# Optimization experiments

Measured on AMD Instinct MI355X. Metric: run time of the kernel, lower is better.

## Reference

```python
import jax, jax.numpy as jnp
import numpy as np

N_NODES = 100000
N_EDGES = 1600000
N_FEAT = 32


def setup_inputs() -> dict:
    key = jax.random.key(0)
    k1, k2, k3, k4 = jax.random.split(key, 4)
    u = jax.random.normal(k1, (N_NODES, N_FEAT), dtype=jnp.float32)
    weights = jax.random.uniform(k2, (N_EDGES,), dtype=jnp.float32)
    row = jax.random.randint(k3, (N_EDGES,), 0, N_NODES)
    col = jax.random.randint(k4, (N_EDGES,), 0, N_NODES)
    edge_index = jnp.stack([row, col]).astype(jnp.int64)
    return {"u": u, "weights": weights, "edge_index": edge_index}


def reference(u, weights, edge_index):
    # row, col: [E]; u: [N, F]; weights: [E]
    row, col = edge_index[0], edge_index[1]
    diff = u[col] - u[row]                      # [E, F] edge gather + diff
    weighted_diff = weights[:, None] * diff     # [E, F]
    # scatter-add into node outputs (index_add_ on row)
    laplacian = jax.ops.segment_sum(weighted_diff, row, num_segments=u.shape[0])
    return laplacian
```

## Files before the change

### kernel.cpp

```cpp
#include <hip/hip_runtime.h>


#define NFEAT 32
#define BUCKET_BITS 7
#define HB 128
#define MAXNB 1024
#define CH 4096
#define HCAP 2560
#define HBLK 64

typedef float nfloat4 __attribute__((ext_vector_type(4)));
typedef unsigned int nuint2 __attribute__((ext_vector_type(2)));

__device__ __forceinline__ float4 nt_load_f4(const float4* p) {
    nfloat4 v = __builtin_nontemporal_load((const nfloat4*)p);
    return make_float4(v.x, v.y, v.z, v.w);
}
__device__ __forceinline__ void nt_store_f4(float4* p, float4 v) {
    nfloat4 t = {v.x, v.y, v.z, v.w};
    __builtin_nontemporal_store(t, (nfloat4*)p);
}
__device__ __forceinline__ uint2 nt_load_u2(const uint2* p) {
    nuint2 v = __builtin_nontemporal_load((const nuint2*)p);
    uint2 r; r.x = v.x; r.y = v.y; return r;
}

__device__ __forceinline__ int wave_incl_scan(int v, int lane) {
#pragma unroll
    for (int off = 1; off < 64; off <<= 1) {
        int t = __shfl_up(v, off, 64);
        if (lane >= off) v += t;
    }
    return v;
}

__global__ __launch_bounds__(512) void conv_hist_kernel(const float4* __restrict__ u4,
                                                        ushort4* __restrict__ ub, int n4,
                                                        const int* __restrict__ row,
                                                        int* __restrict__ hist_part,
                                                        int E, int convBlocks) {
    __shared__ int h[MAXNB];
    if ((int)blockIdx.x < convBlocks) {
        int i = blockIdx.x * 512 + threadIdx.x;
        if (i >= n4) return;
        float4 v = nt_load_f4(&u4[i]);
        ushort4 o;
        unsigned x;
        x = __float_as_uint(v.x); x += 0x7fffu + ((x >> 16) & 1u); o.x = (unsigned short)(x >> 16);
        x = __float_as_uint(v.y); x += 0x7fffu + ((x >> 16) & 1u); o.y = (unsigned short)(x >> 16);
        x = __float_as_uint(v.z); x += 0x7fffu + ((x >> 16) & 1u); o.z = (unsigned short)(x >> 16);
        x = __float_as_uint(v.w); x += 0x7fffu + ((x >> 16) & 1u); o.w = (unsigned short)(x >> 16);
        ub[i] = o;
    } else {
        int hb = blockIdx.x - convBlocks;
        for (int i = threadIdx.x; i < MAXNB; i += 512) h[i] = 0;
        __syncthreads();
        int stride = HBLK * 512;
        for (int e = hb * 512 + threadIdx.x; e < E; e += stride)
            atomicAdd(&h[__builtin_nontemporal_load(&row[e]) >> BUCKET_BITS], 1);
        __syncthreads();
        int* dst = hist_part + (size_t)hb * MAXNB;
        for (int i = threadIdx.x; i < MAXNB; i += 512) dst[i] = h[i];
    }
}

__global__ __launch_bounds__(512) void scan_offsets_kernel(const int* __restrict__ hist_part,
                                                           int* __restrict__ offsets,
                                                           int* __restrict__ cursor) {
    __shared__ int wsum[8];
    int t = threadIdx.x;
    int lane = t & 63, wid = t >> 6;
    int c0 = 0, c1 = 0;
    for (int p = 0; p < HBLK; ++p) {
        const int2* src = (const int2*)(hist_part + (size_t)p * MAXNB);
        int2 v = src[t];
        c0 += v.x; c1 += v.y;
    }
    int pair = c0 + c1;
    int incl = wave_incl_scan(pair, lane);
    if (lane == 63) wsum[wid] = incl;
    __syncthreads();
    int base = 0;
#pragma unroll
    for (int i = 0; i < 8; ++i) { int v = wsum[i]; if (i < wid) base += v; }
    incl += base;
    int excl = incl - pair;
    offsets[2 * t] = excl;
    cursor[2 * t] = excl;
    offsets[2 * t + 1] = excl + c0;
    cursor[2 * t + 1] = excl + c0;
    if (t == 511) offsets[MAXNB] = incl;
}

__global__ __launch_bounds__(512) void fill_sort_kernel(const int* __restrict__ row,
                                                        const int* __restrict__ col,
                                                        const float* __restrict__ w,
                                                        int* __restrict__ cursor,
                                                        uint2* __restrict__ csr,
                                                        int E) {
    __shared__ int hist[MAXNB];
    __shared__ int sc[MAXNB];
    __shared__ int gb0[MAXNB];
    __shared__ int wsum[8];
    __shared__ uint2 so[CH];
    __shared__ unsigned short sbs[CH];

    int tid = threadIdx.x;
    int lane = tid & 63, wid = tid >> 6;
    int lo = blockIdx.x * CH;
    int n = min(E - lo, CH);
    bool full = (n == CH);

    hist[tid] = 0;
    hist[tid + 512] = 0;
    __syncthreads();

    int rst[CH / 512];
    if (full) {
#pragma unroll
        for (int k = 0; k < CH / 512; ++k) {
            int r = __builtin_nontemporal_load(&row[lo + tid + k * 512]);
            rst[k] = r;
            atomicAdd(&hist[r >> BUCKET_BITS], 1);
        }
    } else {
        for (int i = tid; i < n; i += 512)
            atomicAdd(&hist[__builtin_nontemporal_load(&row[lo + i]) >> BUCKET_BITS], 1);
    }
    __syncthreads();

    int c0 = hist[2 * tid];
    int c1 = hist[2 * tid + 1];
    int pair = c0 + c1;
    int incl = wave_incl_scan(pair, lane);
    if (lane == 63) wsum[wid] = incl;
    __syncthreads();
    int base = 0;
#pragma unroll
    for (int i = 0; i < 8; ++i) { int v = wsum[i]; if (i < wid) base += v; }
    incl += base;
    int excl = incl - pair;
    sc[2 * tid] = excl;
    sc[2 * tid + 1] = excl + c0;

    int g0 = c0 ? atomicAdd(&cursor[2 * tid], c0) : 0;
    int g1 = c1 ? atomicAdd(&cursor[2 * tid + 1], c1) : 0;
    gb0[2 * tid] = g0;
    gb0[2 * tid + 1] = g1;
    hist[2 * tid] = g0;
    hist[2 * tid + 1] = g1;
    __syncthreads();

    if (full) {
#pragma unroll
        for (int k = 0; k < CH / 512; ++k) {
            int i = tid + k * 512;
            int r = rst[k];
            unsigned c = (unsigned)__builtin_nontemporal_load(&col[lo + i]);
            float wt = __builtin_nontemporal_load(&w[lo + i]);
            int b = r >> BUCKET_BITS;
            uint2 p;
            p.x = ((unsigned)(r & (HB - 1)) << 25) | c;
            p.y = __float_as_uint(wt);
            int d = atomicAdd(&hist[b], 1);
            int pos = sc[b] + (d - gb0[b]);
            so[pos] = p;
            sbs[pos] = (unsigned short)b;
        }
    } else {
        for (int i = tid; i < n; i += 512) {
            int r = __builtin_nontemporal_load(&row[lo + i]);
            unsigned c = (unsigned)__builtin_nontemporal_load(&col[lo + i]);
            float wt = __builtin_nontemporal_load(&w[lo + i]);
            int b = r >> BUCKET_BITS;
            uint2 p;
            p.x = ((unsigned)(r & (HB - 1)) << 25) | c;
            p.y = __float_as_uint(wt);
            int d = atomicAdd(&hist[b], 1);
            int pos = sc[b] + (d - gb0[b]);
            so[pos] = p;
            sbs[pos] = (unsigned short)b;
        }
    }
    __syncthreads();

    for (int i = tid; i < n; i += 512) {
        int b = sbs[i];
        csr[gb0[b] + (i - sc[b])] = so[i];
    }
}

__global__ __launch_bounds__(512) void node_half_kernel(const ushort4* __restrict__ ub,
                                                        const float4* __restrict__ u4,
                                                        const int* __restrict__ offsets,
                                                        const uint2* __restrict__ csr,
                                                        float4* __restrict__ out4, int N) {
    __shared__ uint2 se[HCAP];
    __shared__ int hist[HB];
    __shared__ int starts[HB + 1];
    __shared__ int sc[HB];

    int b = blockIdx.x;
    int tid = threadIdx.x;
    int start = offsets[b];
    int end = offsets[b + 1];
    int cnt = end - start;

    if (tid < HB) hist[tid] = 0;
    __syncthreads();

    if (cnt <= HCAP) {
        for (int i = start + tid; i < end; i += 512)
            atomicAdd(&hist[nt_load_u2(&csr[i]).x >> 25], 1);
        __syncthreads();
        int myc = (tid < HB) ? hist[tid] : 0;
        int lane = tid & 63;
        int incl = wave_incl_scan(myc, lane);
        if (lane == 63) sc[tid >> 6] = incl;
        __syncthreads();
        if (tid < HB) {
            if (tid >= 64) incl += sc[0];
            int excl = incl - myc;
            starts[tid] = excl;
            hist[tid] = excl;
            if (tid == HB - 1) starts[HB] = incl;
        }
        __syncthreads();
        for (int i = start + tid; i < end; i += 512) {
            uint2 p = nt_load_u2(&csr[i]);
            int pos = atomicAdd(&hist[p.x >> 25], 1);
            se[pos] = p;
        }
        __syncthreads();
        int wave = tid >> 6;
        int f4 = lane & 7;
        int slot = lane >> 3;
        for (int node = wave; node < HB; node += 8) {
            int s0 = starts[node];
            int s1 = starts[node + 1];
            float4 acc = make_float4(0.f, 0.f, 0.f, 0.f);
            float ws_ = 0.f;
            for (int i = s0 + slot; i < s1; i += 8) {
                uint2 p = se[i];
                int c = (int)(p.x & 0x01FFFFFFu);
                float wt = __uint_as_float(p.y);
                ushort4 us = ub[(size_t)c * 8 + f4];
                acc.x += wt * __uint_as_float((unsigned)us.x << 16);
                acc.y += wt * __uint_as_float((unsigned)us.y << 16);
                acc.z += wt * __uint_as_float((unsigned)us.z << 16);
                acc.w += wt * __uint_as_float((unsigned)us.w << 16);
                ws_ += wt;
            }
#pragma unroll
            for (int m = 8; m < 64; m <<= 1) {
                acc.x += __shfl_xor(acc.x, m, 64);
                acc.y += __shfl_xor(acc.y, m, 64);
                acc.z += __shfl_xor(acc.z, m, 64);
                acc.w += __shfl_xor(acc.w, m, 64);
                ws_   += __shfl_xor(ws_,   m, 64);
            }
            int glob = b * HB + node;
            if (slot == 0 && glob < N) {
                float4 ur = nt_load_f4(&u4[(size_t)glob * 8 + f4]);
                float4 o;
                o.x = acc.x - ws_ * ur.x;
                o.y = acc.y - ws_ * ur.y;
                o.z = acc.z - ws_ * ur.z;
                o.w = acc.w - ws_ * ur.w;
                nt_store_f4(&out4[(size_t)glob * 8 + f4], o);
            }
        }
    } else {
        float* tile = (float*)se;
        float* wsumf = (float*)sc;
        for (int i = tid; i < HB * NFEAT; i += 512) tile[i] = 0.f;
        if (tid < HB) wsumf[tid] = 0.f;
        __syncthreads();
        int f4 = tid & 7;
        for (int i = start + (tid >> 3); i < end; i += 64) {
            uint2 p = nt_load_u2(&csr[i]);
            int rl = (int)(p.x >> 25);
            int c = (int)(p.x & 0x01FFFFFFu);
            float wt = __uint_as_float(p.y);
            ushort4 us = ub[(size_t)c * 8 + f4];
            float* t = &tile[rl * NFEAT + f4 * 4];
            atomicAdd(t + 0, wt * __uint_as_float((unsigned)us.x << 16));
            atomicAdd(t + 1, wt * __uint_as_float((unsigned)us.y << 16));
            atomicAdd(t + 2, wt * __uint_as_float((unsigned)us.z << 16));
            atomicAdd(t + 3, wt * __uint_as_float((unsigned)us.w << 16));
            if (f4 == 0) atomicAdd(&wsumf[rl], wt);
        }
        __syncthreads();
#pragma unroll
        for (int pass = 0; pass < 2; ++pass) {
            int idx = pass * 512 + tid;
            int node = idx >> 3;
            int ff = idx & 7;
            int glob = b * HB + node;
            if (glob < N) {
                float4 ur = nt_load_f4(&u4[(size_t)glob * 8 + ff]);
                float ws_ = wsumf[node];
                const float* t = &tile[node * NFEAT + ff * 4];
                float4 o;
                o.x = t[0] - ws_ * ur.x;
                o.y = t[1] - ws_ * ur.y;
                o.z = t[2] - ws_ * ur.z;
                o.w = t[3] - ws_ * ur.w;
                nt_store_f4(&out4[(size_t)glob * 8 + ff], o);
            }
        }
    }
}


__global__ __launch_bounds__(256) void zero_out_kernel(float* __restrict__ out, int n) {
    int i = blockIdx.x * blockDim.x + threadIdx.x;
    if (i < n) out[i] = 0.0f;
}

__global__ __launch_bounds__(256) void scatter_lap_kernel(const float4* __restrict__ u4,
                                                          const float* __restrict__ w,
                                                          const int* __restrict__ row,
                                                          const int* __restrict__ col,
                                                          float* __restrict__ out, int n_edges) {
    int tid = blockIdx.x * blockDim.x + threadIdx.x;
    int e = tid >> 3;
    int f4 = tid & 7;
    if (e >= n_edges) return;
    int r = row[e];
    int c = col[e];
    float wt = w[e];
    float4 uc = u4[(size_t)c * 8 + f4];
    float4 ur = u4[(size_t)r * 8 + f4];
    float* o = out + (size_t)r * NFEAT + f4 * 4;
    atomicAdd(o + 0, wt * (uc.x - ur.x));
    atomicAdd(o + 1, wt * (uc.y - ur.y));
    atomicAdd(o + 2, wt * (uc.z - ur.z));
    atomicAdd(o + 3, wt * (uc.w - ur.w));
}

extern "C" void kernel_launch(void* const* d_in, const int* in_sizes, int n_in,
                              void* d_out, int out_size, void* d_ws, size_t ws_size,
                              hipStream_t stream) {
    const float* u = (const float*)d_in[0];
    const float* w = (const float*)d_in[1];
    const int* ei = (const int*)d_in[2];
    float* out = (float*)d_out;

    const int E = in_sizes[1];
    const int N = out_size / NFEAT;
    const int* row = ei;
    const int* col = ei + E;

    const int NBH = (N + HB - 1) >> BUCKET_BITS;

    const size_t histPartOff = 0;
    const size_t histPartBytes = ((size_t)HBLK * MAXNB * 4 + 255) & ~(size_t)255;
    const size_t offsetsOff = histPartOff + histPartBytes;
    const size_t offsetsBytes = ((size_t)(MAXNB + 1) * 4 + 255) & ~(size_t)255;
    const size_t cursorOff = offsetsOff + offsetsBytes;
    const size_t cursorBytes = ((size_t)MAXNB * 4 + 255) & ~(size_t)255;
    const size_t csrOff = cursorOff + cursorBytes;
    const size_t csrBytes = ((size_t)E * 8 + 255) & ~(size_t)255;
    const size_t ubOff = csrOff + csrBytes;
    const size_t ubBytes = ((size_t)N * NFEAT * 2 + 255) & ~(size_t)255;
    const size_t totalWs = ubOff + ubBytes;

    if (ws_size < totalWs || NBH > MAXNB - 1) {
        zero_out_kernel<<<(out_size + 255) / 256, 256, 0, stream>>>(out, out_size);
        long long threads_total = (long long)E * 8;
        scatter_lap_kernel<<<(unsigned)((threads_total + 255) / 256), 256, 0, stream>>>(
            (const float4*)u, w, row, col, out, E);
        return;
    }

    char* ws = (char*)d_ws;
    int* hist_part = (int*)(ws + histPartOff);
    int* offsets = (int*)(ws + offsetsOff);
    int* cursor = (int*)(ws + cursorOff);
    uint2* csr = (uint2*)(ws + csrOff);
    ushort4* ub = (ushort4*)(ws + ubOff);

    int n4 = N * (NFEAT / 4);
    int convBlocks = (n4 + 511) / 512;
    conv_hist_kernel<<<convBlocks + HBLK, 512, 0, stream>>>((const float4*)u, ub, n4,
                                                            row, hist_part, E, convBlocks);

    scan_offsets_kernel<<<1, 512, 0, stream>>>(hist_part, offsets, cursor);

    const int nChunks = (E + CH - 1) / CH;
    fill_sort_kernel<<<nChunks, 512, 0, stream>>>(row, col, w, cursor, csr, E);

    node_half_kernel<<<NBH, 512, 0, stream>>>(ub, (const float4*)u, offsets, csr,
                                              (float4*)out, N);
}
```

Measured before the change: 172.5 us.

## Fold offset scan and bf16 conversion into fill kernel, cache CSR slice in LDS

Drops the single-block scan kernel. Every fill_sort block now sums the 64 partial histograms and scans them redundantly to get global bucket offsets, and uses zeroed ticket counters in place of a precomputed cursor. The fp32-to-bf16 conversion of u moves from the histogram launch into the fill kernel's prologue, split evenly across its blocks. The node kernel stages its CSR slice in shared memory so the edge records are read from global memory once instead of twice, at the cost of doubling that kernel's LDS use and each fill block re-reading 256KB of partial histograms.

```diff
diff --git a/kernel.cpp b/kernel.cpp
--- a/kernel.cpp
+++ b/kernel.cpp
@@ -34,74 +34,41 @@
     return v;
 }
 
-__global__ __launch_bounds__(512) void conv_hist_kernel(const float4* __restrict__ u4,
-                                                        ushort4* __restrict__ ub, int n4,
-                                                        const int* __restrict__ row,
-                                                        int* __restrict__ hist_part,
-                                                        int E, int convBlocks) {
+__global__ __launch_bounds__(512) void hist_kernel(const int* __restrict__ row,
+                                                   int* __restrict__ hist_part,
+                                                   int* __restrict__ ticket,
+                                                   int E) {
     __shared__ int h[MAXNB];
-    if ((int)blockIdx.x < convBlocks) {
-        int i = blockIdx.x * 512 + threadIdx.x;
-        if (i >= n4) return;
-        float4 v = nt_load_f4(&u4[i]);
-        ushort4 o;
-        unsigned x;
-        x = __float_as_uint(v.x); x += 0x7fffu + ((x >> 16) & 1u); o.x = (unsigned short)(x >> 16);
-        x = __float_as_uint(v.y); x += 0x7fffu + ((x >> 16) & 1u); o.y = (unsigned short)(x >> 16);
-        x = __float_as_uint(v.z); x += 0x7fffu + ((x >> 16) & 1u); o.z = (unsigned short)(x >> 16);
-        x = __float_as_uint(v.w); x += 0x7fffu + ((x >> 16) & 1u); o.w = (unsigned short)(x >> 16);
-        ub[i] = o;
-    } else {
-        int hb = blockIdx.x - convBlocks;
-        for (int i = threadIdx.x; i < MAXNB; i += 512) h[i] = 0;
-        __syncthreads();
-        int stride = HBLK * 512;
-        for (int e = hb * 512 + threadIdx.x; e < E; e += stride)
-            atomicAdd(&h[__builtin_nontemporal_load(&row[e]) >> BUCKET_BITS], 1);
-        __syncthreads();
-        int* dst = hist_part + (size_t)hb * MAXNB;
-        for (int i = threadIdx.x; i < MAXNB; i += 512) dst[i] = h[i];
-    }
-}
-
-__global__ __launch_bounds__(512) void scan_offsets_kernel(const int* __restrict__ hist_part,
-                                                           int* __restrict__ offsets,
-                                                           int* __restrict__ cursor) {
-    __shared__ int wsum[8];
-    int t = threadIdx.x;
-    int lane = t & 63, wid = t >> 6;
-    int c0 = 0, c1 = 0;
-    for (int p = 0; p < HBLK; ++p) {
-        const int2* src = (const int2*)(hist_part + (size_t)p * MAXNB);
-        int2 v = src[t];
-        c0 += v.x; c1 += v.y;
-    }
-    int pair = c0 + c1;
-    int incl = wave_incl_scan(pair, lane);
-    if (lane == 63) wsum[wid] = incl;
-    __syncthreads();
-    int base = 0;
-#pragma unroll
-    for (int i = 0; i < 8; ++i) { int v = wsum[i]; if (i < wid) base += v; }
-    incl += base;
-    int excl = incl - pair;
-    offsets[2 * t] = excl;
-    cursor[2 * t] = excl;
-    offsets[2 * t + 1] = excl + c0;
-    cursor[2 * t + 1] = excl + c0;
-    if (t == 511) offsets[MAXNB] = incl;
+    int hb = blockIdx.x;
+    if (hb == 0) {
+        ticket[threadIdx.x] = 0;
+        ticket[threadIdx.x + 512] = 0;
+    }
+    for (int i = threadIdx.x; i < MAXNB; i += 512) h[i] = 0;
+    __syncthreads();
+    int stride = HBLK * 512;
+    for (int e = hb * 512 + threadIdx.x; e < E; e += stride)
+        atomicAdd(&h[__builtin_nontemporal_load(&row[e]) >> BUCKET_BITS], 1);
+    __syncthreads();
+    int* dst = hist_part + (size_t)hb * MAXNB;
+    for (int i = threadIdx.x; i < MAXNB; i += 512) dst[i] = h[i];
 }
 
 __global__ __launch_bounds__(512) void fill_sort_kernel(const int* __restrict__ row,
                                                         const int* __restrict__ col,
                                                         const float* __restrict__ w,
-                                                        int* __restrict__ cursor,
+                                                        const int* __restrict__ hist_part,
+                                                        int* __restrict__ ticket,
+                                                        int* __restrict__ offsets,
                                                         uint2* __restrict__ csr,
-                                                        int E) {
+                                                        const float4* __restrict__ u4,
+                                                        ushort4* __restrict__ ub,
+                                                        int n4, int E) {
     __shared__ int hist[MAXNB];
     __shared__ int sc[MAXNB];
     __shared__ int gb0[MAXNB];
-    __shared__ int wsum[8];
+    __shared__ int wsumL[8];
+    __shared__ int wsumG[8];
     __shared__ uint2 so[CH];
     __shared__ unsigned short sbs[CH];
 
@@ -111,6 +78,22 @@
     int n = min(E - lo, CH);
     bool full = (n == CH);
 
+    {
+        int per = (n4 + (int)gridDim.x - 1) / (int)gridDim.x;
+        int cb = blockIdx.x * per;
+        int ce = min(n4, cb + per);
+        for (int i = cb + tid; i < ce; i += 512) {
+            float4 v = nt_load_f4(&u4[i]);
+            ushort4 o;
+            unsigned x;
+            x = __float_as_uint(v.x); x += 0x7fffu + ((x >> 16) & 1u); o.x = (unsigned short)(x >> 16);
+            x = __float_as_uint(v.y); x += 0x7fffu + ((x >> 16) & 1u); o.y = (unsigned short)(x >> 16);
+            x = __float_as_uint(v.z); x += 0x7fffu + ((x >> 16) & 1u); o.z = (unsigned short)(x >> 16);
+            x = __float_as_uint(v.w); x += 0x7fffu + ((x >> 16) & 1u); o.w = (unsigned short)(x >> 16);
+            ub[i] = o;
+        }
+    }
+
     hist[tid] = 0;
     hist[tid + 512] = 0;
     __syncthreads();
@@ -127,24 +110,44 @@
         for (int i = tid; i < n; i += 512)
             atomicAdd(&hist[__builtin_nontemporal_load(&row[lo + i]) >> BUCKET_BITS], 1);
     }
+
+    int c0g = 0, c1g = 0;
+    for (int p = 0; p < HBLK; ++p) {
+        int2 v = ((const int2*)(hist_part + (size_t)p * MAXNB))[tid];
+        c0g += v.x; c1g += v.y;
+    }
     __syncthreads();
 
     int c0 = hist[2 * tid];
     int c1 = hist[2 * tid + 1];
-    int pair = c0 + c1;
-    int incl = wave_incl_scan(pair, lane);
-    if (lane == 63) wsum[wid] = incl;
-    __syncthreads();
-    int base = 0;
-#pragma unroll
-    for (int i = 0; i < 8; ++i) { int v = wsum[i]; if (i < wid) base += v; }
-    incl += base;
-    int excl = incl - pair;
-    sc[2 * tid] = excl;
-    sc[2 * tid + 1] = excl + c0;
-
-    int g0 = c0 ? atomicAdd(&cursor[2 * tid], c0) : 0;
-    int g1 = c1 ? atomicAdd(&cursor[2 * tid + 1], c1) : 0;
+    int pairL = c0 + c1;
+    int pairG = c0g + c1g;
+    int inclL = wave_incl_scan(pairL, lane);
+    int inclG = wave_incl_scan(pairG, lane);
+    if (lane == 63) { wsumL[wid] = inclL; wsumG[wid] = inclG; }
+    __syncthreads();
+    int baseL = 0, baseG = 0;
+#pragma unroll
+    for (int i = 0; i < 8; ++i) {
+        int vl = wsumL[i], vg = wsumG[i];
+        if (i < wid) { baseL += vl; baseG += vg; }
+    }
+    inclL += baseL;
+    inclG += baseG;
+    int exclL = inclL - pairL;
+    sc[2 * tid] = exclL;
+    sc[2 * tid + 1] = exclL + c0;
+    int gE0 = inclG - pairG;
+    int gE1 = gE0 + c0g;
+
+    if (blockIdx.x == 0) {
+        offsets[2 * tid] = gE0;
+        offsets[2 * tid + 1] = gE1;
+        if (tid == 511) offsets[MAXNB] = inclG;
+    }
+
+    int g0 = gE0 + (c0 ? atomicAdd(&ticket[2 * tid], c0) : 0);
+    int g1 = gE1 + (c1 ? atomicAdd(&ticket[2 * tid + 1], c1) : 0);
     gb0[2 * tid] = g0;
     gb0[2 * tid + 1] = g1;
     hist[2 * tid] = g0;
@@ -195,6 +198,7 @@
                                                         const int* __restrict__ offsets,
                                                         const uint2* __restrict__ csr,
                                                         float4* __restrict__ out4, int N) {
+    __shared__ uint2 sin_[HCAP];
     __shared__ uint2 se[HCAP];
     __shared__ int hist[HB];
     __shared__ int starts[HB + 1];
@@ -210,8 +214,11 @@
     __syncthreads();
 
     if (cnt <= HCAP) {
-        for (int i = start + tid; i < end; i += 512)
-            atomicAdd(&hist[nt_load_u2(&csr[i]).x >> 25], 1);
+        for (int i = start + tid; i < end; i += 512) {
+            uint2 p = nt_load_u2(&csr[i]);
+            sin_[i - start] = p;
+            atomicAdd(&hist[p.x >> 25], 1);
+        }
         __syncthreads();
         int myc = (tid < HB) ? hist[tid] : 0;
         int lane = tid & 63;
@@ -226,8 +233,8 @@
             if (tid == HB - 1) starts[HB] = incl;
         }
         __syncthreads();
-        for (int i = start + tid; i < end; i += 512) {
-            uint2 p = nt_load_u2(&csr[i]);
+        for (int j = tid; j < cnt; j += 512) {
+            uint2 p = sin_[j];
             int pos = atomicAdd(&hist[p.x >> 25], 1);
             se[pos] = p;
         }
@@ -358,9 +365,9 @@
     const size_t histPartBytes = ((size_t)HBLK * MAXNB * 4 + 255) & ~(size_t)255;
     const size_t offsetsOff = histPartOff + histPartBytes;
     const size_t offsetsBytes = ((size_t)(MAXNB + 1) * 4 + 255) & ~(size_t)255;
-    const size_t cursorOff = offsetsOff + offsetsBytes;
-    const size_t cursorBytes = ((size_t)MAXNB * 4 + 255) & ~(size_t)255;
-    const size_t csrOff = cursorOff + cursorBytes;
+    const size_t ticketOff = offsetsOff + offsetsBytes;
+    const size_t ticketBytes = ((size_t)MAXNB * 4 + 255) & ~(size_t)255;
+    const size_t csrOff = ticketOff + ticketBytes;
     const size_t csrBytes = ((size_t)E * 8 + 255) & ~(size_t)255;
     const size_t ubOff = csrOff + csrBytes;
     const size_t ubBytes = ((size_t)N * NFEAT * 2 + 255) & ~(size_t)255;
@@ -377,19 +384,17 @@
     char* ws = (char*)d_ws;
     int* hist_part = (int*)(ws + histPartOff);
     int* offsets = (int*)(ws + offsetsOff);
-    int* cursor = (int*)(ws + cursorOff);
+    int* ticket = (int*)(ws + ticketOff);
     uint2* csr = (uint2*)(ws + csrOff);
     ushort4* ub = (ushort4*)(ws + ubOff);
 
+    hist_kernel<<<HBLK, 512, 0, stream>>>(row, hist_part, ticket, E);
+
     int n4 = N * (NFEAT / 4);
-    int convBlocks = (n4 + 511) / 512;
-    conv_hist_kernel<<<convBlocks + HBLK, 512, 0, stream>>>((const float4*)u, ub, n4,
-                                                            row, hist_part, E, convBlocks);
-
-    scan_offsets_kernel<<<1, 512, 0, stream>>>(hist_part, offsets, cursor);
-
     const int nChunks = (E + CH - 1) / CH;
-    fill_sort_kernel<<<nChunks, 512, 0, stream>>>(row, col, w, cursor, csr, E);
+    fill_sort_kernel<<<nChunks, 512, 0, stream>>>(row, col, w, hist_part, ticket,
+                                                  offsets, csr, (const float4*)u, ub,
+                                                  n4, E);
 
     node_half_kernel<<<NBH, 512, 0, stream>>>(ub, (const float4*)u, offsets, csr,
                                               (float4*)out, N);
```

New measurement: 188.7 us. +9.4%, slower.
